# Kernel optimization log

Measured on AMD Instinct MI355X. Metric: run time of the kernel, lower is better.

Reference implementation:

```python
import jax, jax.numpy as jnp
import numpy as np

JOINT_CHAINS = {'wrist': ['WRJ1', 'WRJ2'], 'index': ['FFJ4', 'FFJ3', 'FFJ2', 'FFJ1'], 'middle': ['MFJ4', 'MFJ3', 'MFJ2', 'MFJ1'], 'ring': ['RFJ4', 'RFJ3', 'RFJ2', 'RFJ1'], 'little': ['LFJ5', 'LFJ4', 'LFJ3', 'LFJ2', 'LFJ1'], 'thumb': ['THJ5', 'THJ4', 'THJ3', 'THJ2', 'THJ1']}
JOINT_NAMES = ['WRJ1', 'WRJ2', 'FFJ4', 'FFJ3', 'FFJ2', 'FFJ1', 'MFJ4', 'MFJ3', 'MFJ2', 'MFJ1', 'RFJ4', 'RFJ3', 'RFJ2', 'RFJ1', 'LFJ5', 'LFJ4', 'LFJ3', 'LFJ2', 'LFJ1', 'THJ5', 'THJ4', 'THJ3', 'THJ2', 'THJ1']
N_JOINTS = 24


def _build_a_norm():
    # Fixed 24-node kinematic-chain graph, undirected, with self loops,
    # symmetric degree normalization (PyG GCNConv default).
    idx = {n: i for i, n in enumerate(JOINT_NAMES)}
    A = np.zeros((N_JOINTS, N_JOINTS), dtype=np.float32)
    for chain in JOINT_CHAINS.values():
        for i in range(len(chain) - 1):
            u, v = idx[chain[i]], idx[chain[i + 1]]
            A[u, v] = 1.0
            A[v, u] = 1.0
    A = A + np.eye(N_JOINTS, dtype=np.float32)  # add self loops
    deg = A.sum(axis=1)
    dinv = 1.0 / np.sqrt(deg)
    return (dinv[:, None] * A * dinv[None, :]).astype(np.float32)


def setup_inputs() -> dict:
    key = jax.random.key(0)
    k1, k2, k3, k4, k5 = jax.random.split(key, 5)
    B, N, Cin, H, O = 8192, N_JOINTS, 64, 256, 256
    return {
        'node_feats': jax.random.normal(k1, (B, N, Cin), dtype=jnp.float32),
        'W1': jax.random.normal(k2, (Cin, H), dtype=jnp.float32) * 0.05,
        'b1': jax.random.normal(k3, (H,), dtype=jnp.float32) * 0.05,
        'W2': jax.random.normal(k4, (H, O), dtype=jnp.float32) * 0.05,
        'b2': jax.random.normal(k5, (O,), dtype=jnp.float32) * 0.05,
        'A_norm': jnp.asarray(_build_a_norm()),
    }


def reference(node_feats, W1, b1, W2, b2, A_norm):
    # GCNConv layer 1: linear then degree-normalized aggregation, then ReLU
    h = jnp.einsum('nm,bmh->bnh', A_norm, node_feats @ W1) + b1  # (B, N, H)
    h = jax.nn.relu(h)
    # GCNConv layer 2
    h = jnp.einsum('nm,bmo->bno', A_norm, h @ W2) + b2  # (B, N, O)
    h = jax.nn.relu(h)
    # global mean pool over the N=24 nodes of each graph
    return h.mean(axis=1)  # (B, O)
```

## Files before the change

kernel.cpp:

```cpp
#include <hip/hip_runtime.h>
#include <stdint.h>


typedef __attribute__((ext_vector_type(8))) __bf16 bf16x8;
typedef __attribute__((ext_vector_type(4))) __bf16 bf16x4;
typedef __attribute__((ext_vector_type(2))) __bf16 bf16x2;
typedef __attribute__((ext_vector_type(4))) float f32x4;

#define SWZ(row, byteoff) ((unsigned)(byteoff) ^ ((((unsigned)(row)) & 7u) << 4))

__global__ void prep_kernel(const float* __restrict__ W1,
                            const float* __restrict__ W2,
                            unsigned char* __restrict__ ws) {
  int t = blockIdx.x * blockDim.x + threadIdx.x;
  bf16x8 v;
  if (t < 2048) {
    int blk = t >> 6, l = t & 63;
    int ks = blk & 1, hf = blk >> 1;
    int h  = hf * 16 + (l & 15);
    int k0 = ks * 32 + (l >> 4) * 8;
#pragma unroll
    for (int j = 0; j < 8; ++j) v[j] = (__bf16)W1[(k0 + j) * 256 + h];
    *(bf16x8*)(ws + t * 16) = v;
  } else if (t < 10240) {
    int t2 = t - 2048;
    int blk = t2 >> 6, l = t2 & 63;
    int ks = blk & 1;
    int c  = (blk >> 1) & 3;
    int of = blk >> 3;
    int o  = of * 16 + (l & 15);
    int f0 = c * 64 + ks * 32 + (l >> 4) * 8;
#pragma unroll
    for (int j = 0; j < 8; ++j) v[j] = (__bf16)W2[(f0 + j) * 256 + o];
    *(bf16x8*)(ws + 32768 + t2 * 16) = v;
  }
}

__launch_bounds__(512, 4)
__global__ void gnn_kernel(const float* __restrict__ X,
                           const float* __restrict__ b1g,
                           const float* __restrict__ b2g,
                           const float* __restrict__ Ag,
                           const unsigned char* __restrict__ ws,
                           float* __restrict__ out) {
  __shared__ __align__(16) unsigned char ldsX[96 * 128];
  __shared__ __align__(16) unsigned char ldsH[96 * 512];
  __shared__ __align__(16) float ldsB1[256];
  __shared__ __align__(16) float ldsB2[256];

  const int tid  = threadIdx.x;
  const int lane = tid & 63;
  const int wid  = tid >> 6;
  const int ow   = wid & 3;
  const int mw   = wid >> 2;
  const int g0   = blockIdx.x * 4;
  const long row0 = (long)g0 * 24;

  if (tid < 256) { ldsB1[tid] = b1g[tid]; ldsB2[tid] = b2g[tid]; }

  const int r16   = lane & 15;
  const int kgrp  = (lane >> 4) * 8;
  const int lbyte = lane * 16;

#pragma unroll
  for (int it = 0; it < 3; ++it) {
    int idx = tid + it * 512;
    int m   = idx >> 4;
    int c4  = (idx & 15) * 4;
    int n   = m - (m / 24) * 24;
    const float* xr = X + (row0 + m) * 64 + c4;
    float wmid = Ag[n * 25];
    float wdn  = (n > 0)  ? Ag[n * 25 - 1] : 0.f;
    float wup  = (n < 23) ? Ag[n * 25 + 1] : 0.f;
    float4 xc = *(const float4*)xr;
    float ax = wmid * xc.x, ay = wmid * xc.y, az = wmid * xc.z, aw = wmid * xc.w;
    if (wdn != 0.f) {
      float4 xd = *(const float4*)(xr - 64);
      ax += wdn * xd.x; ay += wdn * xd.y; az += wdn * xd.z; aw += wdn * xd.w;
    }
    if (wup != 0.f) {
      float4 xu = *(const float4*)(xr + 64);
      ax += wup * xu.x; ay += wup * xu.y; az += wup * xu.z; aw += wup * xu.w;
    }
    bf16x4 p;
    p[0] = (__bf16)ax; p[1] = (__bf16)ay; p[2] = (__bf16)az; p[3] = (__bf16)aw;
    *(bf16x4*)(ldsX + SWZ(m, m * 128 + c4 * 2)) = p;
  }
  __syncthreads();

  f32x4 acc[4][3];
  const f32x4 z4 = {0.f, 0.f, 0.f, 0.f};
#pragma unroll
  for (int i = 0; i < 4; ++i)
#pragma unroll
    for (int j = 0; j < 3; ++j) acc[i][j] = z4;

#pragma unroll
  for (int ks = 0; ks < 2; ++ks) {
    bf16x8 af[4], bf[3];
    int koff = (ks * 32 + kgrp) * 2;
#pragma unroll
    for (int fi = 0; fi < 4; ++fi)
      af[fi] = *(const bf16x8*)(ws + ((((ow * 4 + fi) * 2) + ks) << 10) + lbyte);
#pragma unroll
    for (int fj = 0; fj < 3; ++fj) {
      int m = mw * 48 + fj * 16 + r16;
      bf[fj] = *(const bf16x8*)(ldsX + SWZ(m, m * 128 + koff));
    }
    __builtin_amdgcn_s_setprio(1);
#pragma unroll
    for (int fi = 0; fi < 4; ++fi)
#pragma unroll
      for (int fj = 0; fj < 3; ++fj)
        acc[fi][fj] = __builtin_amdgcn_mfma_f32_16x16x32_bf16(af[fi], bf[fj], acc[fi][fj], 0, 0, 0);
    __builtin_amdgcn_s_setprio(0);
  }

  {
    int hr = (lane >> 4) * 4;
#pragma unroll
    for (int fi = 0; fi < 4; ++fi) {
      int h = ow * 64 + fi * 16 + hr;
      float4 bb = *(const float4*)&ldsB1[h];
#pragma unroll
      for (int fj = 0; fj < 3; ++fj) {
        int m = mw * 48 + fj * 16 + r16;
        f32x4 v = acc[fi][fj];
        bf16x4 p;
        p[0] = (__bf16)fmaxf(v[0] + bb.x, 0.f);
        p[1] = (__bf16)fmaxf(v[1] + bb.y, 0.f);
        p[2] = (__bf16)fmaxf(v[2] + bb.z, 0.f);
        p[3] = (__bf16)fmaxf(v[3] + bb.w, 0.f);
        *(bf16x4*)(ldsH + SWZ(m, m * 512 + h * 2)) = p;
      }
    }
  }
  __syncthreads();

#pragma unroll
  for (int i = 0; i < 4; ++i)
#pragma unroll
    for (int j = 0; j < 3; ++j) acc[i][j] = z4;

  const unsigned char* w2p = ws + 32768;
  bf16x8 afc[4];
#pragma unroll
  for (int fi = 0; fi < 4; ++fi)
    afc[fi] = *(const bf16x8*)(w2p + ((((ow * 4 + fi) * 4 + 0) * 2 + 0) << 10) + lbyte);

#pragma unroll
  for (int s = 0; s < 8; ++s) {
    const int c  = s >> 1;
    const int ks = s & 1;
    bf16x8 afn[4];
    if (s < 7) {
      const int c2  = (s + 1) >> 1;
      const int ks2 = (s + 1) & 1;
#pragma unroll
      for (int fi = 0; fi < 4; ++fi)
        afn[fi] = *(const bf16x8*)(w2p + ((((ow * 4 + fi) * 4 + c2) * 2 + ks2) << 10) + lbyte);
    }
    bf16x8 bf[3];
    int foff = (c * 64 + ks * 32 + kgrp) * 2;
#pragma unroll
    for (int fj = 0; fj < 3; ++fj) {
      int m = mw * 48 + fj * 16 + r16;
      bf[fj] = *(const bf16x8*)(ldsH + SWZ(m, m * 512 + foff));
    }
    __builtin_amdgcn_s_setprio(1);
#pragma unroll
    for (int fi = 0; fi < 4; ++fi)
#pragma unroll
      for (int fj = 0; fj < 3; ++fj)
        acc[fi][fj] = __builtin_amdgcn_mfma_f32_16x16x32_bf16(afc[fi], bf[fj], acc[fi][fj], 0, 0, 0);
    __builtin_amdgcn_s_setprio(0);
#pragma unroll
    for (int fi = 0; fi < 4; ++fi) afc[fi] = afn[fi];
  }
  __syncthreads();

  {
    int orr = (lane >> 4) * 4;
#pragma unroll
    for (int fi = 0; fi < 4; ++fi) {
      int o = ow * 64 + fi * 16 + orr;
#pragma unroll
      for (int fj = 0; fj < 3; ++fj) {
        int m = mw * 48 + fj * 16 + r16;
        f32x4 v = acc[fi][fj];
        bf16x4 p;
        p[0] = (__bf16)v[0]; p[1] = (__bf16)v[1];
        p[2] = (__bf16)v[2]; p[3] = (__bf16)v[3];
        *(bf16x4*)(ldsH + SWZ(m, m * 512 + o * 2)) = p;
      }
    }
  }
  __syncthreads();

  {
    const int g  = wid & 3;
    const int o2 = (wid >> 2) * 128 + lane * 2;
    const int rb = g * 24;
    float bb[2] = { ldsB2[o2], ldsB2[o2 + 1] };
    float s[2]  = {0.f, 0.f};
    float zp[2] = {0.f, 0.f};
    float zc[2], zn[2];
    {
      bf16x2 z = *(const bf16x2*)(ldsH + SWZ(rb, rb * 512 + o2 * 2));
      bf16x2 y = *(const bf16x2*)(ldsH + SWZ(rb + 1, (rb + 1) * 512 + o2 * 2));
      zc[0] = (float)z[0]; zc[1] = (float)z[1];
      zn[0] = (float)y[0]; zn[1] = (float)y[1];
    }
#pragma unroll
    for (int nn = 0; nn < 24; ++nn) {
      const float w0 = Ag[nn * 25];
      float q[2];
#pragma unroll
      for (int j = 0; j < 2; ++j) q[j] = w0 * zc[j] + bb[j];
      if (nn > 0) {
        const float wd = Ag[nn * 25 - 1];
#pragma unroll
        for (int j = 0; j < 2; ++j) q[j] += wd * zp[j];
      }
      if (nn < 23) {
        const float wu = Ag[nn * 25 + 1];
#pragma unroll
        for (int j = 0; j < 2; ++j) q[j] += wu * zn[j];
      }
#pragma unroll
      for (int j = 0; j < 2; ++j) s[j] += fmaxf(q[j], 0.f);
#pragma unroll
      for (int j = 0; j < 2; ++j) { zp[j] = zc[j]; zc[j] = zn[j]; }
      if (nn < 22) {
        int r = rb + nn + 2;
        bf16x2 z = *(const bf16x2*)(ldsH + SWZ(r, r * 512 + o2 * 2));
        zn[0] = (float)z[0]; zn[1] = (float)z[1];
      }
    }
    float2 r2;
    r2.x = s[0] * (1.f / 24.f);
    r2.y = s[1] * (1.f / 24.f);
    *(float2*)(out + (size_t)(g0 + g) * 256 + o2) = r2;
  }
}

extern "C" void kernel_launch(void* const* d_in, const int* in_sizes, int n_in,
                              void* d_out, int out_size, void* d_ws, size_t ws_size,
                              hipStream_t stream) {
  (void)n_in; (void)out_size; (void)ws_size;
  const float* X  = (const float*)d_in[0];
  const float* W1 = (const float*)d_in[1];
  const float* b1 = (const float*)d_in[2];
  const float* W2 = (const float*)d_in[3];
  const float* b2 = (const float*)d_in[4];
  const float* A  = (const float*)d_in[5];
  float* out = (float*)d_out;
  unsigned char* ws = (unsigned char*)d_ws;

  int B = in_sizes[0] / (24 * 64);
  prep_kernel<<<40, 256, 0, stream>>>(W1, W2, ws);
  gnn_kernel<<<B / 4, 512, 0, stream>>>(X, b1, b2, A, ws, out);
}
```

Before: 58.38 us.

## Fuse layer-2 aggregation and mean pooling into MFMA register epilogue

Swaps the MFMA operand order in the second GEMM so each lane holds four consecutive node rows for one output column. The layer-2 adjacency aggregation, bias, ReLU and mean pool then run directly on registers, using cross-lane shuffles for neighbour rows and xor-shuffles for the per-graph reduction. This removes the bf16 round-trip through LDS, two block barriers and the serial 24-step per-thread loop. Adjacency coefficients are cached in LDS tables. The cost is more shuffles and per-lane branching logic, and the output store pattern changes to scalar writes.

```diff
diff --git a/kernel.cpp b/kernel.cpp
--- a/kernel.cpp
+++ b/kernel.cpp
@@ -4,7 +4,6 @@
 
 typedef __attribute__((ext_vector_type(8))) __bf16 bf16x8;
 typedef __attribute__((ext_vector_type(4))) __bf16 bf16x4;
-typedef __attribute__((ext_vector_type(2))) __bf16 bf16x2;
 typedef __attribute__((ext_vector_type(4))) float f32x4;
 
 #define SWZ(row, byteoff) ((unsigned)(byteoff) ^ ((((unsigned)(row)) & 7u) << 4))
@@ -47,6 +46,9 @@
   __shared__ __align__(16) unsigned char ldsH[96 * 512];
   __shared__ __align__(16) float ldsB1[256];
   __shared__ __align__(16) float ldsB2[256];
+  __shared__ __align__(16) float wdT[24];
+  __shared__ __align__(16) float w0T[24];
+  __shared__ __align__(16) float wuT[24];
 
   const int tid  = threadIdx.x;
   const int lane = tid & 63;
@@ -57,6 +59,11 @@
   const long row0 = (long)g0 * 24;
 
   if (tid < 256) { ldsB1[tid] = b1g[tid]; ldsB2[tid] = b2g[tid]; }
+  if (tid < 24) {
+    wdT[tid] = tid > 0  ? Ag[tid * 25 - 1] : 0.f;
+    w0T[tid] = Ag[tid * 25];
+    wuT[tid] = tid < 23 ? Ag[tid * 25 + 1] : 0.f;
+  }
 
   const int r16   = lane & 15;
   const int kgrp  = (lane >> 4) * 8;
@@ -137,10 +144,11 @@
   }
   __syncthreads();
 
-#pragma unroll
-  for (int i = 0; i < 4; ++i)
-#pragma unroll
-    for (int j = 0; j < 3; ++j) acc[i][j] = z4;
+  f32x4 acc2[3][4];
+#pragma unroll
+  for (int j = 0; j < 3; ++j)
+#pragma unroll
+    for (int i = 0; i < 4; ++i) acc2[j][i] = z4;
 
   const unsigned char* w2p = ws + 32768;
   bf16x8 afc[4];
@@ -169,78 +177,57 @@
     }
     __builtin_amdgcn_s_setprio(1);
 #pragma unroll
-    for (int fi = 0; fi < 4; ++fi)
-#pragma unroll
-      for (int fj = 0; fj < 3; ++fj)
-        acc[fi][fj] = __builtin_amdgcn_mfma_f32_16x16x32_bf16(afc[fi], bf[fj], acc[fi][fj], 0, 0, 0);
+    for (int fj = 0; fj < 3; ++fj)
+#pragma unroll
+      for (int fi = 0; fi < 4; ++fi)
+        acc2[fj][fi] = __builtin_amdgcn_mfma_f32_16x16x32_bf16(bf[fj], afc[fi], acc2[fj][fi], 0, 0, 0);
     __builtin_amdgcn_s_setprio(0);
 #pragma unroll
     for (int fi = 0; fi < 4; ++fi) afc[fi] = afn[fi];
   }
-  __syncthreads();
 
   {
-    int orr = (lane >> 4) * 4;
+    const int grp = lane >> 4;
+    const int l16 = lane & 15;
+    const int src_up = (lane - 16) & 63;
+    const int src_dn = (lane + 16) & 63;
 #pragma unroll
     for (int fi = 0; fi < 4; ++fi) {
-      int o = ow * 64 + fi * 16 + orr;
+      const int o = ow * 64 + fi * 16 + l16;
+      const float b2v = ldsB2[o];
+      float s3[3], s0[3];
 #pragma unroll
       for (int fj = 0; fj < 3; ++fj) {
-        int m = mw * 48 + fj * 16 + r16;
-        f32x4 v = acc[fi][fj];
-        bf16x4 p;
-        p[0] = (__bf16)v[0]; p[1] = (__bf16)v[1];
-        p[2] = (__bf16)v[2]; p[3] = (__bf16)v[3];
-        *(bf16x4*)(ldsH + SWZ(m, m * 512 + o * 2)) = p;
+        s3[fj] = __shfl(acc2[fj][fi][3], src_up);
+        s0[fj] = __shfl(acc2[fj][fi][0], src_dn);
       }
-    }
-  }
-  __syncthreads();
-
-  {
-    const int g  = wid & 3;
-    const int o2 = (wid >> 2) * 128 + lane * 2;
-    const int rb = g * 24;
-    float bb[2] = { ldsB2[o2], ldsB2[o2 + 1] };
-    float s[2]  = {0.f, 0.f};
-    float zp[2] = {0.f, 0.f};
-    float zc[2], zn[2];
-    {
-      bf16x2 z = *(const bf16x2*)(ldsH + SWZ(rb, rb * 512 + o2 * 2));
-      bf16x2 y = *(const bf16x2*)(ldsH + SWZ(rb + 1, (rb + 1) * 512 + o2 * 2));
-      zc[0] = (float)z[0]; zc[1] = (float)z[1];
-      zn[0] = (float)y[0]; zn[1] = (float)y[1];
-    }
-#pragma unroll
-    for (int nn = 0; nn < 24; ++nn) {
-      const float w0 = Ag[nn * 25];
-      float q[2];
-#pragma unroll
-      for (int j = 0; j < 2; ++j) q[j] = w0 * zc[j] + bb[j];
-      if (nn > 0) {
-        const float wd = Ag[nn * 25 - 1];
-#pragma unroll
-        for (int j = 0; j < 2; ++j) q[j] += wd * zp[j];
+      float p0 = 0.f, p1 = 0.f;
+#pragma unroll
+      for (int fj = 0; fj < 3; ++fj) {
+        const int lmb = fj * 16 + grp * 4;
+        const int nb  = (lmb < 24) ? lmb : lmb - 24;
+        f32x4 wd4 = *(const f32x4*)&wdT[nb];
+        f32x4 w04 = *(const f32x4*)&w0T[nb];
+        f32x4 wu4 = *(const f32x4*)&wuT[nb];
+        f32x4 v = acc2[fj][fi];
+        float zl0 = s3[fj], zr3 = s0[fj];
+        if (fj > 0 && grp == 0) zl0 = s3[fj - 1];
+        if (fj < 2 && grp == 3) zr3 = s0[fj + 1];
+        float q0 = b2v + wd4[0] * zl0 + w04[0] * v[0] + wu4[0] * v[1];
+        float q1 = b2v + wd4[1] * v[0] + w04[1] * v[1] + wu4[1] * v[2];
+        float q2 = b2v + wd4[2] * v[1] + w04[2] * v[2] + wu4[2] * v[3];
+        float q3 = b2v + wd4[3] * v[2] + w04[3] * v[3] + wu4[3] * zr3;
+        float qs = fmaxf(q0, 0.f) + fmaxf(q1, 0.f) +
+                   fmaxf(q2, 0.f) + fmaxf(q3, 0.f);
+        if (fj == 0) p0 += qs;
+        else if (fj == 2) p1 += qs;
+        else { bool low = grp < 2; p0 += low ? qs : 0.f; p1 += low ? 0.f : qs; }
       }
-      if (nn < 23) {
-        const float wu = Ag[nn * 25 + 1];
-#pragma unroll
-        for (int j = 0; j < 2; ++j) q[j] += wu * zn[j];
-      }
-#pragma unroll
-      for (int j = 0; j < 2; ++j) s[j] += fmaxf(q[j], 0.f);
-#pragma unroll
-      for (int j = 0; j < 2; ++j) { zp[j] = zc[j]; zc[j] = zn[j]; }
-      if (nn < 22) {
-        int r = rb + nn + 2;
-        bf16x2 z = *(const bf16x2*)(ldsH + SWZ(r, r * 512 + o2 * 2));
-        zn[0] = (float)z[0]; zn[1] = (float)z[1];
-      }
-    }
-    float2 r2;
-    r2.x = s[0] * (1.f / 24.f);
-    r2.y = s[1] * (1.f / 24.f);
-    *(float2*)(out + (size_t)(g0 + g) * 256 + o2) = r2;
+      p0 += __shfl_xor(p0, 16); p0 += __shfl_xor(p0, 32);
+      p1 += __shfl_xor(p1, 16); p1 += __shfl_xor(p1, 32);
+      if (grp == 0) out[(size_t)(g0 + 2 * mw)     * 256 + o] = p0 * (1.f / 24.f);
+      if (grp == 1) out[(size_t)(g0 + 2 * mw + 1) * 256 + o] = p1 * (1.f / 24.f);
+    }
   }
 }
 
```

After: 57.00 us. -2.4%, faster.
